# Kernel tuning notes

Hardware: AMD Instinct MI355X
Metric: run time of the kernel (lower is better)

Reference implementation:

```python
import jax, jax.numpy as jnp
import numpy as np


def lstm_encode(x, Wih, Whh, b):
    """x: [S, T, F] -> final hidden state [S, H]. PyTorch LSTM gate order (i, f, g, o)."""
    S = x.shape[0]
    H = Whh.shape[1]

    def step(carry, xt):
        h, c = carry
        z = xt @ Wih.T + h @ Whh.T + b  # [S, 4H]
        i, f, g, o = jnp.split(z, 4, axis=-1)
        c = jax.nn.sigmoid(f) * c + jax.nn.sigmoid(i) * jnp.tanh(g)
        h = jax.nn.sigmoid(o) * jnp.tanh(c)
        return (h, c), None

    init = (jnp.zeros((S, H), x.dtype), jnp.zeros((S, H), x.dtype))
    (h, _), _ = jax.lax.scan(step, init, jnp.swapaxes(x, 0, 1))
    return h


def gatv2(h, Ws, Wd, a, bias):
    """Dense GATv2 on batched fully-connected graphs (no self loops).
    h: [G, N, Hin]; Ws, Wd: [nh, Hin, O]; a: [nh, O]; bias: [nh, O] -> [G, N, nh, O].
    Graph is fully connected (all i != j), so edge-softmax == dense row softmax
    with the diagonal masked out; this is the efficient dense form of the
    gather / LeakyReLU / edge-softmax / scatter pattern in DGL's GATv2Conv."""
    nh = Ws.shape[0]
    N = h.shape[1]
    self_mask = jnp.eye(N, dtype=bool)
    outs = []
    for hd in range(nh):  # small fixed head count; loop caps peak memory
        fs = h @ Ws[hd]  # [G, N, O] source-projected feats (messages)
        fd = h @ Wd[hd]  # [G, N, O] dst-projected feats
        e = jax.nn.leaky_relu(fd[:, :, None, :] + fs[:, None, :, :], 0.2)  # [G, dst, src, O]
        logits = jnp.where(self_mask, -jnp.inf, e @ a[hd])  # [G, dst, src]
        attn = jax.nn.softmax(logits, axis=-1)
        outs.append(jnp.einsum('gds,gso->gdo', attn, fs) + bias[hd])
    return jnp.stack(outs, axis=2)


def cosine(x, y, eps=1e-6):
    xn = x / jnp.maximum(jnp.linalg.norm(x, axis=-1, keepdims=True), eps)
    yn = y / jnp.maximum(jnp.linalg.norm(y, axis=-1, keepdims=True), eps)
    return (xn * yn).sum(-1)


def setup_inputs() -> dict:
    key = jax.random.key(0)
    B, K, T, N, F, H, GH, NH = 16, 4, 64, 128, 16, 32, 32, 8
    ks = jax.random.split(key, 16)

    def rn(k, shape, scale=1.0):
        return jax.random.normal(k, shape, jnp.float32) * scale

    return {
        'anchor': rn(ks[0], (B, T, N, F)),
        'pos': rn(ks[1], (B, T, N, F)),
        'neg': rn(ks[2], (B, K, T, N, F)),
        'hideout': rn(ks[3], (B, 2)),
        'timestep': jax.random.uniform(ks[4], (B, 1), jnp.float32),
        'Wih': rn(ks[5], (4 * H, F), 1.0 / np.sqrt(F)),
        'Whh': rn(ks[6], (4 * H, H), 1.0 / np.sqrt(H)),
        'b_lstm': rn(ks[7], (4 * H,), 0.1),
        'W1s': rn(ks[8], (NH, H, H), 1.0 / np.sqrt(H)),
        'W1d': rn(ks[9], (NH, H, H), 1.0 / np.sqrt(H)),
        'a1': rn(ks[10], (NH, H), 1.0 / np.sqrt(H)),
        'b1': rn(ks[11], (NH, H), 0.1),
        'W2s': rn(ks[12], (1, H, GH), 1.0 / np.sqrt(H)),
        'W2d': rn(ks[13], (1, H, GH), 1.0 / np.sqrt(H)),
        'a2': rn(ks[14], (1, GH), 1.0 / np.sqrt(GH)),
        'b2': rn(ks[15], (1, GH), 0.1),
        'num_agents': 128,
    }


def reference(anchor, pos, neg, hideout, timestep, Wih, Whh, b_lstm,
              W1s, W1d, a1, b1, W2s, W2d, a2, b2, num_agents):
    B, T, N, F = anchor.shape
    K = neg.shape[1]
    H = Whh.shape[1]
    # per-agent time series -> LSTM sequences
    a_seq = jnp.transpose(anchor, (0, 2, 1, 3)).reshape(B * N, T, F)
    p_seq = jnp.transpose(pos, (0, 2, 1, 3)).reshape(B * N, T, F)
    n_seq = jnp.transpose(neg, (0, 1, 3, 2, 4)).reshape(B * K * N, T, F)
    hn = lstm_encode(jnp.concatenate([a_seq, p_seq, n_seq], 0), Wih, Whh, b_lstm)
    hg = hn.reshape(-1, N, H)  # [(2+K)*B, N, H] batched fully-connected graphs
    h1 = gatv2(hg, W1s, W1d, a1, b1).mean(axis=2)  # mean over 8 heads
    h2 = gatv2(h1, W2s, W2d, a2, b2)[:, :, 0, :]   # single head, squeezed
    pooled = h2.mean(axis=1)                        # AvgPooling over nodes
    anchor_res = pooled[:B]
    pos_res = pooled[B:2 * B]
    neg_res = pooled[2 * B:].reshape(B, K, -1)
    sim_pos = cosine(anchor_res, pos_res)[:, None]      # [B, 1]
    sim_neg = cosine(anchor_res[:, None, :], neg_res)   # [B, K]
    all_vecs = jnp.concatenate([sim_neg, sim_pos], axis=1)  # positive last
    contrastive = (-jax.nn.log_softmax(all_vecs, axis=1)[:, -1]).mean()
    res = jnp.concatenate([anchor_res, hideout, timestep], axis=-1)
    return res, contrastive
```

## Files before the change

kernel.cpp:

```cpp
#include <hip/hip_runtime.h>
#include <math.h>


typedef __bf16 bf16x8 __attribute__((ext_vector_type(8)));
typedef float  f32x4  __attribute__((ext_vector_type(4)));
typedef unsigned int u32x4 __attribute__((ext_vector_type(4)));

__device__ __forceinline__ float fast_rcp(float x) { return __builtin_amdgcn_rcpf(x); }
__device__ __forceinline__ float sigm(float x)     { return fast_rcp(1.f + __expf(-x)); }
__device__ __forceinline__ float tanh_fast(float x){ return fmaf(2.f, fast_rcp(1.f + __expf(-2.f * x)), -1.f); }

#define KEEP4(x) asm volatile("" : "+v"(x))

__global__ __launch_bounds__(256, 1) void lstm_mfma_kernel(
    const float* __restrict__ anchor, const float* __restrict__ pos,
    const float* __restrict__ neg, const float* __restrict__ Wih,
    const float* __restrict__ Whh, const float* __restrict__ bias,
    float* __restrict__ hn)
{
    __shared__ unsigned int Hbuf[2][2][512];
    const int tid  = threadIdx.x;
    const int pair = tid >> 7;
    const int wid  = (tid >> 6) & 1;
    const int lane = tid & 63;
    const int l15  = lane & 15;
    const int g4   = lane >> 4;

    for (int i = tid; i < 2048; i += 256) ((unsigned int*)Hbuf)[i] = 0u;

    u32x4 whhH[4], whhL[4], wihH[4];
    float bq[4];
    #pragma unroll
    for (int G = 0; G < 4; ++G) {
        const int c = G * 32 + wid * 16 + l15;
        bq[G] = bias[c];
        union { u32x4 u; bf16x8 v; } th, tl, ti;
        const float* wr = Whh + c * 32 + g4 * 8;
        #pragma unroll
        for (int i = 0; i < 8; ++i) {
            float wv = wr[i];
            __bf16 hi = (__bf16)wv;
            th.v[i] = hi;
            tl.v[i] = (__bf16)(wv - (float)hi);
        }
        if (g4 < 2) {
            const float* wr2 = Wih + c * 16 + g4 * 8;
            #pragma unroll
            for (int i = 0; i < 8; ++i) ti.v[i] = (__bf16)wr2[i];
        } else {
            #pragma unroll
            for (int i = 0; i < 8; ++i) ti.v[i] = (__bf16)0.f;
        }
        whhH[G] = th.u; whhL[G] = tl.u; wihH[G] = ti.u;
    }
    #pragma unroll
    for (int G = 0; G < 4; ++G) { KEEP4(whhH[G]); KEEP4(whhL[G]); KEEP4(wihH[G]); }

    const int s = blockIdx.x * 32 + pair * 16 + l15;
    const float* xbase; int sl;
    if (s < 2048)      { xbase = anchor; sl = s; }
    else if (s < 4096) { xbase = pos;    sl = s - 2048; }
    else               { xbase = neg;    sl = s - 4096; }
    const bool xact = (g4 < 2);
    const float* xp = xbase + (sl >> 7) * 131072 + (sl & 127) * 16 + (xact ? g4 * 8 : 0);

    const float4 z4 = make_float4(0.f, 0.f, 0.f, 0.f);
    float4 xaA = z4, xbA = z4, xaB = z4, xbB = z4;
    if (xact) {
        xaA = *(const float4*)(xp);        xbA = *(const float4*)(xp + 4);
        xaB = *(const float4*)(xp + 2048); xbB = *(const float4*)(xp + 2052);
    }

    float cst[4] = {0,0,0,0};
    float hv[4]  = {0,0,0,0};

    const int c0  = g4 * 2;
    const int swz = (l15 & 3) << 1;
    const int ro0 = l15 * 32 + ((c0 ^ swz) << 2);
    const int ro1 = l15 * 32 + (((c0 + 1) ^ swz) << 2);
    const int jw  = wid * 16 + l15;
    unsigned int* buf0 = Hbuf[pair][0];
    unsigned int* buf1 = Hbuf[pair][1];
    int cur = 0;
    __syncthreads();

    #define LSTM_STEP(XA, XB)                                                          \
    {                                                                                  \
        const unsigned int* rb = cur ? buf1 : buf0;                                    \
        unsigned int*       wb = cur ? buf0 : buf1;                                    \
        bf16x8 ax;                                                                     \
        ax[0]=(__bf16)XA.x; ax[1]=(__bf16)XA.y; ax[2]=(__bf16)XA.z; ax[3]=(__bf16)XA.w;\
        ax[4]=(__bf16)XB.x; ax[5]=(__bf16)XB.y; ax[6]=(__bf16)XB.z; ax[7]=(__bf16)XB.w;\
        uint4 v0 = *(const uint4*)(rb + ro0);                                          \
        uint4 v1 = *(const uint4*)(rb + ro1);                                          \
        union { unsigned int u[4]; bf16x8 v; } ahi;                                    \
        ahi.u[0] = __builtin_amdgcn_perm(v0.y, v0.x, 0x05040100u);                     \
        ahi.u[1] = __builtin_amdgcn_perm(v0.w, v0.z, 0x05040100u);                     \
        ahi.u[2] = __builtin_amdgcn_perm(v1.y, v1.x, 0x05040100u);                     \
        ahi.u[3] = __builtin_amdgcn_perm(v1.w, v1.z, 0x05040100u);                     \
        f32x4 z[4];                                                                    \
        _Pragma("unroll")                                                              \
        for (int G = 0; G < 4; ++G) {                                                  \
            f32x4 a = __builtin_amdgcn_mfma_f32_16x16x32_bf16(                         \
                ax, __builtin_bit_cast(bf16x8, wihH[G]), (f32x4)(0.f), 0, 0, 0);       \
            a = __builtin_amdgcn_mfma_f32_16x16x32_bf16(                               \
                ahi.v, __builtin_bit_cast(bf16x8, whhH[G]), a, 0, 0, 0);               \
            a = __builtin_amdgcn_mfma_f32_16x16x32_bf16(                               \
                ahi.v, __builtin_bit_cast(bf16x8, whhL[G]), a, 0, 0, 0);               \
            z[G] = a;                                                                  \
        }                                                                              \
        _Pragma("unroll")                                                              \
        for (int r = 0; r < 4; ++r) {                                                  \
            float zi = z[0][r] + bq[0];                                                \
            float zf = z[1][r] + bq[1];                                                \
            float zg = z[2][r] + bq[2];                                                \
            float zo = z[3][r] + bq[3];                                                \
            float cn = fmaf(sigm(zf), cst[r], sigm(zi) * tanh_fast(zg));               \
            cst[r] = cn;                                                               \
            float h = sigm(zo) * tanh_fast(cn);                                        \
            hv[r] = h;                                                                 \
            unsigned int pk = (unsigned int)__builtin_bit_cast(unsigned short,         \
                                                               (__bf16)h);            \
            const int mm = g4 * 4 + r;                                                 \
            wb[mm * 32 + (((jw >> 2) ^ ((mm & 3) << 1)) << 2) + (jw & 3)] = pk;        \
        }                                                                              \
        __syncthreads();                                                               \
        cur ^= 1;                                                                      \
    }

    for (int t = 0; t < 64; t += 2) {
        float4 cA1 = xaA, cA2 = xbA;
        if (xact && t + 2 < 64) {
            const float* p = xp + (t + 2) * 2048;
            xaA = *(const float4*)(p); xbA = *(const float4*)(p + 4);
        }
        LSTM_STEP(cA1, cA2);

        float4 cB1 = xaB, cB2 = xbB;
        if (xact && t + 3 < 64) {
            const float* p = xp + (t + 3) * 2048;
            xaB = *(const float4*)(p); xbB = *(const float4*)(p + 4);
        }
        LSTM_STEP(cB1, cB2);
    }
    #undef LSTM_STEP

    const int seq0 = blockIdx.x * 32 + pair * 16;
    #pragma unroll
    for (int r = 0; r < 4; ++r) {
        hn[(seq0 + g4 * 4 + r) * 32 + jw] = hv[r];
    }
}

__device__ __forceinline__ int fsoff(int n) { return n * 36 + ((n >> 5) << 2); }

__global__ __launch_bounds__(256) void gat1_kernel(
    const float* __restrict__ hn, const float* __restrict__ W1s,
    const float* __restrict__ W1d, const float* __restrict__ a1,
    const float* __restrict__ b1, float* __restrict__ h1heads)
{
    const int g = blockIdx.x >> 4, hd = (blockIdx.x >> 1) & 7, half = blockIdx.x & 1;
    const int dbase = half << 6;
    __shared__ float FSf[128 * 36 + 16];
    __shared__ float FD[64][36];
    __shared__ float AVr[32];
    __shared__ float As06[128];
    __shared__ float Ad06[64];
    const int tid = threadIdx.x;

    if (tid < 32) AVr[tid] = a1[hd * 32 + tid];

    {
        const int o = tid & 31, nb = tid >> 5;
        const bool own = (nb >> 2) == half;
        float wcs[32];
        const float* wsp = W1s + hd * 1024 + o;
        #pragma unroll
        for (int k = 0; k < 32; ++k) wcs[k] = wsp[k * 32];
        const float* hp = hn + g * 4096 + nb * 512;
        if (own) {
            float wcd[32];
            const float* wdp = W1d + hd * 1024 + o;
            #pragma unroll
            for (int k = 0; k < 32; ++k) wcd[k] = wdp[k * 32];
            #pragma unroll 1
            for (int n = 0; n < 16; ++n) {
                const int row = nb * 16 + n;
                float a0 = 0.f, a1_ = 0.f, b0 = 0.f, b1_ = 0.f;
                #pragma unroll
                for (int k0 = 0; k0 < 32; k0 += 4) {
                    float4 hv = *(const float4*)(hp + n * 32 + k0);
                    a0 = fmaf(hv.x, wcs[k0+0], a0); b0 = fmaf(hv.x, wcd[k0+0], b0);
                    a1_ = fmaf(hv.y, wcs[k0+1], a1_); b1_ = fmaf(hv.y, wcd[k0+1], b1_);
                    a0 = fmaf(hv.z, wcs[k0+2], a0); b0 = fmaf(hv.z, wcd[k0+2], b0);
                    a1_ = fmaf(hv.w, wcs[k0+3], a1_); b1_ = fmaf(hv.w, wcd[k0+3], b1_);
                }
                FSf[fsoff(row) + o] = a0 + a1_;
                FD[row - dbase][o] = b0 + b1_;
            }
        } else {
            #pragma unroll 1
            for (int n = 0; n < 16; ++n) {
                const int row = nb * 16 + n;
                float a0 = 0.f, a1_ = 0.f;
                #pragma unroll
                for (int k0 = 0; k0 < 32; k0 += 4) {
                    float4 hv = *(const float4*)(hp + n * 32 + k0);
                    a0 = fmaf(hv.x, wcs[k0+0], a0);
                    a1_ = fmaf(hv.y, wcs[k0+1], a1_);
                    a0 = fmaf(hv.z, wcs[k0+2], a0);
                    a1_ = fmaf(hv.w, wcs[k0+3], a1_);
                }
                FSf[fsoff(row) + o] = a0 + a1_;
            }
        }
    }
    __syncthreads();

    if (tid < 128) {
        float ss = 0.f;
        const float* fr = FSf + fsoff(tid);
        #pragma unroll
        for (int oo = 0; oo < 32; ++oo) {
            int o = (oo + tid) & 31;
            ss = fmaf(AVr[o], fr[o], ss);
        }
        As06[tid] = 0.6f * ss;
    } else if (tid < 192) {
        const int dl = tid - 128;
        float sd = 0.f;
        #pragma unroll
        for (int oo = 0; oo < 32; ++oo) {
            int o = (oo + dl) & 31;
            sd = fmaf(AVr[o], FD[dl][o], sd);
        }
        Ad06[dl] = 0.6f * sd;
    }
    __syncthreads();

    const int dl = tid >> 2, d = dbase + dl, sq = tid & 3, sbase = sq << 5;
    float fdr[32], avs[32];
    #pragma unroll
    for (int c = 0; c < 8; ++c) {
        float4 v = *(const float4*)&FD[dl][c * 4];
        fdr[c*4+0] = v.x; fdr[c*4+1] = v.y; fdr[c*4+2] = v.z; fdr[c*4+3] = v.w;
        float4 wv = *(const float4*)&AVr[c * 4];
        avs[c*4+0] = 0.4f * wv.x; avs[c*4+1] = 0.4f * wv.y;
        avs[c*4+2] = 0.4f * wv.z; avs[c*4+3] = 0.4f * wv.w;
    }
    const float adc = Ad06[dl];

    float Z = 0.f;
    float acc[32];
    #pragma unroll
    for (int o = 0; o < 32; ++o) acc[o] = 0.f;
    #pragma unroll 1
    for (int si = 0; si < 32; ++si) {
        const int s = sbase + si;
        const float* fr = FSf + fsoff(s);
        float4 fa[8];
        #pragma unroll
        for (int c = 0; c < 8; ++c) fa[c] = *(const float4*)(fr + c * 4);
        float c0 = 0.f, c1 = 0.f, c2 = 0.f, c3 = 0.f;
        #pragma unroll
        for (int c = 0; c < 8; ++c) {
            float e0 = fdr[c*4+0] + fa[c].x; c0 = fmaf(avs[c*4+0], __builtin_fabsf(e0), c0);
            float e1 = fdr[c*4+1] + fa[c].y; c1 = fmaf(avs[c*4+1], __builtin_fabsf(e1), c1);
            float e2 = fdr[c*4+2] + fa[c].z; c2 = fmaf(avs[c*4+2], __builtin_fabsf(e2), c2);
            float e3 = fdr[c*4+3] + fa[c].w; c3 = fmaf(avs[c*4+3], __builtin_fabsf(e3), c3);
        }
        float v = adc + As06[s] + ((c0 + c1) + (c2 + c3));
        float e = (s == d) ? 0.f : __expf(v);
        Z += e;
        #pragma unroll
        for (int c = 0; c < 8; ++c) {
            acc[c*4+0] = fmaf(e, fa[c].x, acc[c*4+0]);
            acc[c*4+1] = fmaf(e, fa[c].y, acc[c*4+1]);
            acc[c*4+2] = fmaf(e, fa[c].z, acc[c*4+2]);
            acc[c*4+3] = fmaf(e, fa[c].w, acc[c*4+3]);
        }
    }
    Z += __shfl_xor(Z, 1); Z += __shfl_xor(Z, 2);
    const float rz = fast_rcp(Z);
    #pragma unroll
    for (int o = 0; o < 32; ++o) {
        acc[o] += __shfl_xor(acc[o], 1);
        acc[o] += __shfl_xor(acc[o], 2);
    }

    if (sq == 0) {
        float* dst = h1heads + ((size_t)((g * 8 + hd) * 128 + d)) * 32;
        const float* bp = b1 + hd * 32;
        #pragma unroll
        for (int c = 0; c < 8; ++c) {
            float4 v;
            v.x = fmaf(acc[c*4+0], rz, bp[c*4+0]);
            v.y = fmaf(acc[c*4+1], rz, bp[c*4+1]);
            v.z = fmaf(acc[c*4+2], rz, bp[c*4+2]);
            v.w = fmaf(acc[c*4+3], rz, bp[c*4+3]);
            *(float4*)(dst + c * 4) = v;
        }
    }
}

__global__ __launch_bounds__(256) void gat2_kernel(
    const float* __restrict__ h1heads, const float* __restrict__ W2s,
    const float* __restrict__ W2d, const float* __restrict__ a2,
    const float* __restrict__ b2, float* __restrict__ pooled)
{
    const int g = blockIdx.x;
    __shared__ float HS[128][36];
    __shared__ float FSf[128 * 36 + 16];
    __shared__ float FD[128][36];
    __shared__ float AVr[32];
    __shared__ float As06[128];
    __shared__ float Ad06[128];
    const int tid = threadIdx.x;

    if (tid < 32) AVr[tid] = a2[tid];

    {
        #pragma unroll
        for (int i = 0; i < 4; ++i) {
            int idx4 = i * 256 + tid;
            float sx = 0.f, sy = 0.f, sz = 0.f, sw = 0.f;
            #pragma unroll
            for (int hdd = 0; hdd < 8; ++hdd) {
                const float4* src = (const float4*)(h1heads + (size_t)(g * 8 + hdd) * 4096);
                float4 v = src[idx4];
                sx += v.x; sy += v.y; sz += v.z; sw += v.w;
            }
            int n = idx4 >> 3, k0 = (idx4 & 7) * 4;
            float4 r; r.x = sx * 0.125f; r.y = sy * 0.125f; r.z = sz * 0.125f; r.w = sw * 0.125f;
            *(float4*)&HS[n][k0] = r;
        }
    }
    __syncthreads();

    {
        const int o = tid & 31, nb = tid >> 5;
        float wcs[32], wcd[32];
        const float* wsp = W2s + o;
        const float* wdp = W2d + o;
        #pragma unroll
        for (int k = 0; k < 32; ++k) { wcs[k] = wsp[k * 32]; wcd[k] = wdp[k * 32]; }
        #pragma unroll 1
        for (int n = nb * 16; n < nb * 16 + 16; ++n) {
            float a0 = 0.f, a1_ = 0.f, b0 = 0.f, b1_ = 0.f;
            #pragma unroll
            for (int k0 = 0; k0 < 32; k0 += 4) {
                const float4 hv = *(const float4*)&HS[n][k0];
                a0 = fmaf(hv.x, wcs[k0+0], a0); b0 = fmaf(hv.x, wcd[k0+0], b0);
                a1_ = fmaf(hv.y, wcs[k0+1], a1_); b1_ = fmaf(hv.y, wcd[k0+1], b1_);
                a0 = fmaf(hv.z, wcs[k0+2], a0); b0 = fmaf(hv.z, wcd[k0+2], b0);
                a1_ = fmaf(hv.w, wcs[k0+3], a1_); b1_ = fmaf(hv.w, wcd[k0+3], b1_);
            }
            FSf[fsoff(n) + o] = a0 + a1_;
            FD[n][o] = b0 + b1_;
        }
    }
    __syncthreads();

    if (tid < 128) {
        float ss = 0.f, sd = 0.f;
        const float* fr = FSf + fsoff(tid);
        #pragma unroll
        for (int oo = 0; oo < 32; ++oo) {
            int o = (oo + tid) & 31;
            float a = AVr[o];
            ss = fmaf(a, fr[o], ss);
            sd = fmaf(a, FD[tid][o], sd);
        }
        As06[tid] = 0.6f * ss;
        Ad06[tid] = 0.6f * sd;
    }
    __syncthreads();

    const int d = tid >> 1, sbase = (tid & 1) << 6;
    float fdr[32], avs[32];
    #pragma unroll
    for (int c = 0; c < 8; ++c) {
        float4 v = *(const float4*)&FD[d][c * 4];
        fdr[c*4+0] = v.x; fdr[c*4+1] = v.y; fdr[c*4+2] = v.z; fdr[c*4+3] = v.w;
        float4 wv = *(const float4*)&AVr[c * 4];
        avs[c*4+0] = 0.4f * wv.x; avs[c*4+1] = 0.4f * wv.y;
        avs[c*4+2] = 0.4f * wv.z; avs[c*4+3] = 0.4f * wv.w;
    }
    const float adc = Ad06[d];

    float Z = 0.f;
    float acc[32];
    #pragma unroll
    for (int o = 0; o < 32; ++o) acc[o] = 0.f;
    #pragma unroll 1
    for (int si = 0; si < 64; ++si) {
        const int s = sbase + si;
        const float* fr = FSf + fsoff(s);
        float4 fa[8];
        #pragma unroll
        for (int c = 0; c < 8; ++c) fa[c] = *(const float4*)(fr + c * 4);
        float c0 = 0.f, c1 = 0.f, c2 = 0.f, c3 = 0.f;
        #pragma unroll
        for (int c = 0; c < 8; ++c) {
            float e0 = fdr[c*4+0] + fa[c].x; c0 = fmaf(avs[c*4+0], __builtin_fabsf(e0), c0);
            float e1 = fdr[c*4+1] + fa[c].y; c1 = fmaf(avs[c*4+1], __builtin_fabsf(e1), c1);
            float e2 = fdr[c*4+2] + fa[c].z; c2 = fmaf(avs[c*4+2], __builtin_fabsf(e2), c2);
            float e3 = fdr[c*4+3] + fa[c].w; c3 = fmaf(avs[c*4+3], __builtin_fabsf(e3), c3);
        }
        float v = adc + As06[s] + ((c0 + c1) + (c2 + c3));
        float e = (s == d) ? 0.f : __expf(v);
        Z += e;
        #pragma unroll
        for (int c = 0; c < 8; ++c) {
            acc[c*4+0] = fmaf(e, fa[c].x, acc[c*4+0]);
            acc[c*4+1] = fmaf(e, fa[c].y, acc[c*4+1]);
            acc[c*4+2] = fmaf(e, fa[c].z, acc[c*4+2]);
            acc[c*4+3] = fmaf(e, fa[c].w, acc[c*4+3]);
        }
    }
    Z += __shfl_xor(Z, 1);
    const float rz = fast_rcp(Z);
    #pragma unroll
    for (int o = 0; o < 32; ++o) acc[o] += __shfl_xor(acc[o], 1);

    __syncthreads();
    if ((tid & 1) == 0) {
        #pragma unroll
        for (int c = 0; c < 4; ++c) {
            float4 v;
            v.x = acc[c*4+0] * rz; v.y = acc[c*4+1] * rz;
            v.z = acc[c*4+2] * rz; v.w = acc[c*4+3] * rz;
            *(float4*)&FD[d][c * 4] = v;
        }
    } else {
        #pragma unroll
        for (int c = 4; c < 8; ++c) {
            float4 v;
            v.x = acc[c*4+0] * rz; v.y = acc[c*4+1] * rz;
            v.z = acc[c*4+2] * rz; v.w = acc[c*4+3] * rz;
            *(float4*)&FD[d][c * 4] = v;
        }
    }
    __syncthreads();

    if (tid < 32) {
        float sp = 0.f;
        #pragma unroll 1
        for (int n = 0; n < 128; ++n) sp += FD[n][tid];
        pooled[g * 32 + tid] = fmaf(sp, 1.f / 128.f, b2[tid]);
    }
}

__global__ void final_kernel(const float* __restrict__ pooled,
                             const float* __restrict__ hideout,
                             const float* __restrict__ timestep,
                             float* __restrict__ out)
{
    const int b = threadIdx.x;
    __shared__ float lossArr[16];
    if (b < 16) {
        const float* A  = pooled + b * 32;
        const float* Pv = pooled + (16 + b) * 32;
        float av[32];
        float na = 0.f;
        #pragma unroll
        for (int i = 0; i < 32; ++i) { av[i] = A[i]; na += av[i] * av[i]; }
        float npv = 0.f, dp = 0.f;
        #pragma unroll
        for (int i = 0; i < 32; ++i) { float p = Pv[i]; npv += p * p; dp += av[i] * p; }
        const float eps = 1e-6f;
        const float ia = 1.f / fmaxf(sqrtf(na), eps);
        const float sp = dp * ia / fmaxf(sqrtf(npv), eps);
        float sn[4];
        #pragma unroll
        for (int k = 0; k < 4; ++k) {
            const float* Nv = pooled + (32 + b * 4 + k) * 32;
            float nn = 0.f, dn = 0.f;
            #pragma unroll
            for (int i = 0; i < 32; ++i) { float q = Nv[i]; nn += q * q; dn += av[i] * q; }
            sn[k] = dn * ia / fmaxf(sqrtf(nn), eps);
        }
        float m = sp;
        #pragma unroll
        for (int k = 0; k < 4; ++k) m = fmaxf(m, sn[k]);
        float Z = expf(sp - m);
        #pragma unroll
        for (int k = 0; k < 4; ++k) Z += expf(sn[k] - m);
        lossArr[b] = logf(Z) + m - sp;
        float* r = out + b * 35;
        #pragma unroll
        for (int i = 0; i < 32; ++i) r[i] = av[i];
        r[32] = hideout[b * 2];
        r[33] = hideout[b * 2 + 1];
        r[34] = timestep[b];
    }
    __syncthreads();
    if (b == 0) {
        float s = 0.f;
        #pragma unroll
        for (int i = 0; i < 16; ++i) s += lossArr[i];
        out[560] = s * (1.f / 16.f);
    }
}

extern "C" void kernel_launch(void* const* d_in, const int* in_sizes, int n_in,
                              void* d_out, int out_size, void* d_ws, size_t ws_size,
                              hipStream_t stream) {
    const float* anchor   = (const float*)d_in[0];
    const float* pos      = (const float*)d_in[1];
    const float* neg      = (const float*)d_in[2];
    const float* hideout  = (const float*)d_in[3];
    const float* timestep = (const float*)d_in[4];
    const float* Wih      = (const float*)d_in[5];
    const float* Whh      = (const float*)d_in[6];
    const float* b_lstm   = (const float*)d_in[7];
    const float* W1s      = (const float*)d_in[8];
    const float* W1d      = (const float*)d_in[9];
    const float* a1       = (const float*)d_in[10];
    const float* b1       = (const float*)d_in[11];
    const float* W2s      = (const float*)d_in[12];
    const float* W2d      = (const float*)d_in[13];
    const float* a2       = (const float*)d_in[14];
    const float* b2       = (const float*)d_in[15];
    float* out = (float*)d_out;

    char* ws = (char*)d_ws;
    float* hn      = (float*)(ws);
    float* h1heads = (float*)(ws + 1605632);
    float* pooled  = (float*)(ws + 14188544);

    hipLaunchKernelGGL(lstm_mfma_kernel, dim3(384), dim3(256), 0, stream,
                       anchor, pos, neg, Wih, Whh, b_lstm, hn);
    hipLaunchKernelGGL(gat1_kernel,  dim3(1536), dim3(256), 0, stream,
                       hn, W1s, W1d, a1, b1, h1heads);
    hipLaunchKernelGGL(gat2_kernel,  dim3(96),   dim3(256), 0, stream,
                       h1heads, W2s, W2d, a2, b2, pooled);
    hipLaunchKernelGGL(final_kernel, dim3(1),    dim3(64),  0, stream,
                       pooled, hideout, timestep, out);
}
```

Baseline: 162.1 us.

## Split LSTM blocks to one wave pair and give each GAT1 thread two destinations

The LSTM kernel now runs 128-thread blocks, each holding one pair of waves, across twice as many blocks. Its per-step __syncthreads is replaced by a raw s_barrier preceded by an LDS wait, so the two independent wave pairs that used to share a block no longer stall each other at every timestep. The GAT1 kernel stops splitting destinations into halves: each block handles one (graph, head) and computes both source and destination projections once, and each thread accumulates two destination rows. Each source-feature load is reused twice, and the redundant source projection done by both halves is removed. The cost is higher register pressure in GAT1 (two 32-wide accumulators) and fewer GAT1 blocks.

```diff
diff --git a/kernel.cpp b/kernel.cpp
--- a/kernel.cpp
+++ b/kernel.cpp
@@ -12,21 +12,28 @@
 
 #define KEEP4(x) asm volatile("" : "+v"(x))
 
-__global__ __launch_bounds__(256, 1) void lstm_mfma_kernel(
+#define PAIR_BARRIER() do {                                     \
+    asm volatile("s_waitcnt lgkmcnt(0)" ::: "memory");          \
+    __builtin_amdgcn_sched_barrier(0);                          \
+    __builtin_amdgcn_s_barrier();                               \
+    __builtin_amdgcn_sched_barrier(0);                          \
+} while (0)
+
+__global__ __launch_bounds__(128, 1) void lstm_mfma_kernel(
     const float* __restrict__ anchor, const float* __restrict__ pos,
     const float* __restrict__ neg, const float* __restrict__ Wih,
     const float* __restrict__ Whh, const float* __restrict__ bias,
     float* __restrict__ hn)
 {
-    __shared__ unsigned int Hbuf[2][2][512];
+    __shared__ unsigned int Hbuf[2][512];
     const int tid  = threadIdx.x;
-    const int pair = tid >> 7;
-    const int wid  = (tid >> 6) & 1;
+    const int wid  = tid >> 6;
     const int lane = tid & 63;
     const int l15  = lane & 15;
     const int g4   = lane >> 4;
 
-    for (int i = tid; i < 2048; i += 256) ((unsigned int*)Hbuf)[i] = 0u;
+    #pragma unroll
+    for (int i = 0; i < 8; ++i) ((unsigned int*)Hbuf)[tid + i * 128] = 0u;
 
     u32x4 whhH[4], whhL[4], wihH[4];
     float bq[4];
@@ -56,7 +63,7 @@
     #pragma unroll
     for (int G = 0; G < 4; ++G) { KEEP4(whhH[G]); KEEP4(whhL[G]); KEEP4(wihH[G]); }
 
-    const int s = blockIdx.x * 32 + pair * 16 + l15;
+    const int s = blockIdx.x * 16 + l15;
     const float* xbase; int sl;
     if (s < 2048)      { xbase = anchor; sl = s; }
     else if (s < 4096) { xbase = pos;    sl = s - 2048; }
@@ -79,15 +86,13 @@
     const int ro0 = l15 * 32 + ((c0 ^ swz) << 2);
     const int ro1 = l15 * 32 + (((c0 + 1) ^ swz) << 2);
     const int jw  = wid * 16 + l15;
-    unsigned int* buf0 = Hbuf[pair][0];
-    unsigned int* buf1 = Hbuf[pair][1];
     int cur = 0;
-    __syncthreads();
+    PAIR_BARRIER();
 
     #define LSTM_STEP(XA, XB)                                                          \
     {                                                                                  \
-        const unsigned int* rb = cur ? buf1 : buf0;                                    \
-        unsigned int*       wb = cur ? buf0 : buf1;                                    \
+        const unsigned int* rb = Hbuf[cur];                                            \
+        unsigned int*       wb = Hbuf[cur ^ 1];                                        \
         bf16x8 ax;                                                                     \
         ax[0]=(__bf16)XA.x; ax[1]=(__bf16)XA.y; ax[2]=(__bf16)XA.z; ax[3]=(__bf16)XA.w;\
         ax[4]=(__bf16)XB.x; ax[5]=(__bf16)XB.y; ax[6]=(__bf16)XB.z; ax[7]=(__bf16)XB.w;\
@@ -124,7 +129,7 @@
             const int mm = g4 * 4 + r;                                                 \
             wb[mm * 32 + (((jw >> 2) ^ ((mm & 3) << 1)) << 2) + (jw & 3)] = pk;        \
         }                                                                              \
-        __syncthreads();                                                               \
+        PAIR_BARRIER();                                                                \
         cur ^= 1;                                                                      \
     }
 
@@ -145,7 +150,7 @@
     }
     #undef LSTM_STEP
 
-    const int seq0 = blockIdx.x * 32 + pair * 16;
+    const int seq0 = blockIdx.x * 16;
     #pragma unroll
     for (int r = 0; r < 4; ++r) {
         hn[(seq0 + g4 * 4 + r) * 32 + jw] = hv[r];
@@ -154,106 +159,81 @@
 
 __device__ __forceinline__ int fsoff(int n) { return n * 36 + ((n >> 5) << 2); }
 
-__global__ __launch_bounds__(256) void gat1_kernel(
+__global__ __launch_bounds__(256, 2) void gat1_kernel(
     const float* __restrict__ hn, const float* __restrict__ W1s,
     const float* __restrict__ W1d, const float* __restrict__ a1,
     const float* __restrict__ b1, float* __restrict__ h1heads)
 {
-    const int g = blockIdx.x >> 4, hd = (blockIdx.x >> 1) & 7, half = blockIdx.x & 1;
-    const int dbase = half << 6;
+    const int g = blockIdx.x >> 3, hd = blockIdx.x & 7;
     __shared__ float FSf[128 * 36 + 16];
-    __shared__ float FD[64][36];
+    __shared__ float FD[128][36];
     __shared__ float AVr[32];
     __shared__ float As06[128];
-    __shared__ float Ad06[64];
+    __shared__ float Ad06[128];
     const int tid = threadIdx.x;
 
     if (tid < 32) AVr[tid] = a1[hd * 32 + tid];
 
     {
         const int o = tid & 31, nb = tid >> 5;
-        const bool own = (nb >> 2) == half;
-        float wcs[32];
+        float wcs[32], wcd[32];
         const float* wsp = W1s + hd * 1024 + o;
-        #pragma unroll
-        for (int k = 0; k < 32; ++k) wcs[k] = wsp[k * 32];
+        const float* wdp = W1d + hd * 1024 + o;
+        #pragma unroll
+        for (int k = 0; k < 32; ++k) { wcs[k] = wsp[k * 32]; wcd[k] = wdp[k * 32]; }
         const float* hp = hn + g * 4096 + nb * 512;
-        if (own) {
-            float wcd[32];
-            const float* wdp = W1d + hd * 1024 + o;
+        #pragma unroll 1
+        for (int n = 0; n < 16; ++n) {
+            const int row = nb * 16 + n;
+            float a0 = 0.f, a1_ = 0.f, b0 = 0.f, b1_ = 0.f;
             #pragma unroll
-            for (int k = 0; k < 32; ++k) wcd[k] = wdp[k * 32];
-            #pragma unroll 1
-            for (int n = 0; n < 16; ++n) {
-                const int row = nb * 16 + n;
-                float a0 = 0.f, a1_ = 0.f, b0 = 0.f, b1_ = 0.f;
-                #pragma unroll
-                for (int k0 = 0; k0 < 32; k0 += 4) {
-                    float4 hv = *(const float4*)(hp + n * 32 + k0);
-                    a0 = fmaf(hv.x, wcs[k0+0], a0); b0 = fmaf(hv.x, wcd[k0+0], b0);
-                    a1_ = fmaf(hv.y, wcs[k0+1], a1_); b1_ = fmaf(hv.y, wcd[k0+1], b1_);
-                    a0 = fmaf(hv.z, wcs[k0+2], a0); b0 = fmaf(hv.z, wcd[k0+2], b0);
-                    a1_ = fmaf(hv.w, wcs[k0+3], a1_); b1_ = fmaf(hv.w, wcd[k0+3], b1_);
-                }
-                FSf[fsoff(row) + o] = a0 + a1_;
-                FD[row - dbase][o] = b0 + b1_;
+            for (int k0 = 0; k0 < 32; k0 += 4) {
+                float4 hv = *(const float4*)(hp + n * 32 + k0);
+                a0 = fmaf(hv.x, wcs[k0+0], a0); b0 = fmaf(hv.x, wcd[k0+0], b0);
+                a1_ = fmaf(hv.y, wcs[k0+1], a1_); b1_ = fmaf(hv.y, wcd[k0+1], b1_);
+                a0 = fmaf(hv.z, wcs[k0+2], a0); b0 = fmaf(hv.z, wcd[k0+2], b0);
+                a1_ = fmaf(hv.w, wcs[k0+3], a1_); b1_ = fmaf(hv.w, wcd[k0+3], b1_);
             }
-        } else {
-            #pragma unroll 1
-            for (int n = 0; n < 16; ++n) {
-                const int row = nb * 16 + n;
-                float a0 = 0.f, a1_ = 0.f;
-                #pragma unroll
-                for (int k0 = 0; k0 < 32; k0 += 4) {
-                    float4 hv = *(const float4*)(hp + n * 32 + k0);
-                    a0 = fmaf(hv.x, wcs[k0+0], a0);
-                    a1_ = fmaf(hv.y, wcs[k0+1], a1_);
-                    a0 = fmaf(hv.z, wcs[k0+2], a0);
-                    a1_ = fmaf(hv.w, wcs[k0+3], a1_);
-                }
-                FSf[fsoff(row) + o] = a0 + a1_;
-            }
+            FSf[fsoff(row) + o] = a0 + a1_;
+            FD[row][o] = b0 + b1_;
         }
     }
     __syncthreads();
 
     if (tid < 128) {
-        float ss = 0.f;
+        float ss = 0.f, sd = 0.f;
         const float* fr = FSf + fsoff(tid);
         #pragma unroll
         for (int oo = 0; oo < 32; ++oo) {
             int o = (oo + tid) & 31;
-            ss = fmaf(AVr[o], fr[o], ss);
+            float a = AVr[o];
+            ss = fmaf(a, fr[o], ss);
+            sd = fmaf(a, FD[tid][o], sd);
         }
         As06[tid] = 0.6f * ss;
-    } else if (tid < 192) {
-        const int dl = tid - 128;
-        float sd = 0.f;
-        #pragma unroll
-        for (int oo = 0; oo < 32; ++oo) {
-            int o = (oo + dl) & 31;
-            sd = fmaf(AVr[o], FD[dl][o], sd);
-        }
-        Ad06[dl] = 0.6f * sd;
-    }
-    __syncthreads();
-
-    const int dl = tid >> 2, d = dbase + dl, sq = tid & 3, sbase = sq << 5;
-    float fdr[32], avs[32];
+        Ad06[tid] = 0.6f * sd;
+    }
+    __syncthreads();
+
+    const int p = tid >> 2, sq = tid & 3, sbase = sq << 5;
+    const int d0 = p, d1 = p + 64;
+    float fdr0[32], fdr1[32], avs[32];
     #pragma unroll
     for (int c = 0; c < 8; ++c) {
-        float4 v = *(const float4*)&FD[dl][c * 4];
-        fdr[c*4+0] = v.x; fdr[c*4+1] = v.y; fdr[c*4+2] = v.z; fdr[c*4+3] = v.w;
+        float4 v0 = *(const float4*)&FD[d0][c * 4];
+        fdr0[c*4+0] = v0.x; fdr0[c*4+1] = v0.y; fdr0[c*4+2] = v0.z; fdr0[c*4+3] = v0.w;
+        float4 v1 = *(const float4*)&FD[d1][c * 4];
+        fdr1[c*4+0] = v1.x; fdr1[c*4+1] = v1.y; fdr1[c*4+2] = v1.z; fdr1[c*4+3] = v1.w;
         float4 wv = *(const float4*)&AVr[c * 4];
         avs[c*4+0] = 0.4f * wv.x; avs[c*4+1] = 0.4f * wv.y;
         avs[c*4+2] = 0.4f * wv.z; avs[c*4+3] = 0.4f * wv.w;
     }
-    const float adc = Ad06[dl];
-
-    float Z = 0.f;
-    float acc[32];
-    #pragma unroll
-    for (int o = 0; o < 32; ++o) acc[o] = 0.f;
+    const float adc0 = Ad06[d0], adc1 = Ad06[d1];
+
+    float Z0 = 0.f, Z1 = 0.f;
+    float acc0[32], acc1[32];
+    #pragma unroll
+    for (int o = 0; o < 32; ++o) { acc0[o] = 0.f; acc1[o] = 0.f; }
     #pragma unroll 1
     for (int si = 0; si < 32; ++si) {
         const int s = sbase + si;
@@ -261,44 +241,66 @@
         float4 fa[8];
         #pragma unroll
         for (int c = 0; c < 8; ++c) fa[c] = *(const float4*)(fr + c * 4);
-        float c0 = 0.f, c1 = 0.f, c2 = 0.f, c3 = 0.f;
+        float c00 = 0.f, c01 = 0.f, c02 = 0.f, c03 = 0.f;
+        float c10 = 0.f, c11 = 0.f, c12 = 0.f, c13 = 0.f;
         #pragma unroll
         for (int c = 0; c < 8; ++c) {
-            float e0 = fdr[c*4+0] + fa[c].x; c0 = fmaf(avs[c*4+0], __builtin_fabsf(e0), c0);
-            float e1 = fdr[c*4+1] + fa[c].y; c1 = fmaf(avs[c*4+1], __builtin_fabsf(e1), c1);
-            float e2 = fdr[c*4+2] + fa[c].z; c2 = fmaf(avs[c*4+2], __builtin_fabsf(e2), c2);
-            float e3 = fdr[c*4+3] + fa[c].w; c3 = fmaf(avs[c*4+3], __builtin_fabsf(e3), c3);
-        }
-        float v = adc + As06[s] + ((c0 + c1) + (c2 + c3));
-        float e = (s == d) ? 0.f : __expf(v);
-        Z += e;
+            float e;
+            e = fdr0[c*4+0] + fa[c].x; c00 = fmaf(avs[c*4+0], __builtin_fabsf(e), c00);
+            e = fdr1[c*4+0] + fa[c].x; c10 = fmaf(avs[c*4+0], __builtin_fabsf(e), c10);
+            e = fdr0[c*4+1] + fa[c].y; c01 = fmaf(avs[c*4+1], __builtin_fabsf(e), c01);
+            e = fdr1[c*4+1] + fa[c].y; c11 = fmaf(avs[c*4+1], __builtin_fabsf(e), c11);
+            e = fdr0[c*4+2] + fa[c].z; c02 = fmaf(avs[c*4+2], __builtin_fabsf(e), c02);
+            e = fdr1[c*4+2] + fa[c].z; c12 = fmaf(avs[c*4+2], __builtin_fabsf(e), c12);
+            e = fdr0[c*4+3] + fa[c].w; c03 = fmaf(avs[c*4+3], __builtin_fabsf(e), c03);
+            e = fdr1[c*4+3] + fa[c].w; c13 = fmaf(avs[c*4+3], __builtin_fabsf(e), c13);
+        }
+        const float ass = As06[s];
+        float v0 = adc0 + ass + ((c00 + c01) + (c02 + c03));
+        float v1 = adc1 + ass + ((c10 + c11) + (c12 + c13));
+        float e0 = (s == d0) ? 0.f : __expf(v0);
+        float e1 = (s == d1) ? 0.f : __expf(v1);
+        Z0 += e0; Z1 += e1;
         #pragma unroll
         for (int c = 0; c < 8; ++c) {
-            acc[c*4+0] = fmaf(e, fa[c].x, acc[c*4+0]);
-            acc[c*4+1] = fmaf(e, fa[c].y, acc[c*4+1]);
-            acc[c*4+2] = fmaf(e, fa[c].z, acc[c*4+2]);
-            acc[c*4+3] = fmaf(e, fa[c].w, acc[c*4+3]);
-        }
-    }
-    Z += __shfl_xor(Z, 1); Z += __shfl_xor(Z, 2);
-    const float rz = fast_rcp(Z);
+            acc0[c*4+0] = fmaf(e0, fa[c].x, acc0[c*4+0]);
+            acc1[c*4+0] = fmaf(e1, fa[c].x, acc1[c*4+0]);
+            acc0[c*4+1] = fmaf(e0, fa[c].y, acc0[c*4+1]);
+            acc1[c*4+1] = fmaf(e1, fa[c].y, acc1[c*4+1]);
+            acc0[c*4+2] = fmaf(e0, fa[c].z, acc0[c*4+2]);
+            acc1[c*4+2] = fmaf(e1, fa[c].z, acc1[c*4+2]);
+            acc0[c*4+3] = fmaf(e0, fa[c].w, acc0[c*4+3]);
+            acc1[c*4+3] = fmaf(e1, fa[c].w, acc1[c*4+3]);
+        }
+    }
+    Z0 += __shfl_xor(Z0, 1); Z0 += __shfl_xor(Z0, 2);
+    Z1 += __shfl_xor(Z1, 1); Z1 += __shfl_xor(Z1, 2);
+    const float rz0 = fast_rcp(Z0), rz1 = fast_rcp(Z1);
     #pragma unroll
     for (int o = 0; o < 32; ++o) {
-        acc[o] += __shfl_xor(acc[o], 1);
-        acc[o] += __shfl_xor(acc[o], 2);
+        acc0[o] += __shfl_xor(acc0[o], 1);
+        acc0[o] += __shfl_xor(acc0[o], 2);
+        acc1[o] += __shfl_xor(acc1[o], 1);
+        acc1[o] += __shfl_xor(acc1[o], 2);
     }
 
     if (sq == 0) {
-        float* dst = h1heads + ((size_t)((g * 8 + hd) * 128 + d)) * 32;
         const float* bp = b1 + hd * 32;
+        float* dst0 = h1heads + ((size_t)((g * 8 + hd) * 128 + d0)) * 32;
+        float* dst1 = h1heads + ((size_t)((g * 8 + hd) * 128 + d1)) * 32;
         #pragma unroll
         for (int c = 0; c < 8; ++c) {
             float4 v;
-            v.x = fmaf(acc[c*4+0], rz, bp[c*4+0]);
-            v.y = fmaf(acc[c*4+1], rz, bp[c*4+1]);
-            v.z = fmaf(acc[c*4+2], rz, bp[c*4+2]);
-            v.w = fmaf(acc[c*4+3], rz, bp[c*4+3]);
-            *(float4*)(dst + c * 4) = v;
+            v.x = fmaf(acc0[c*4+0], rz0, bp[c*4+0]);
+            v.y = fmaf(acc0[c*4+1], rz0, bp[c*4+1]);
+            v.z = fmaf(acc0[c*4+2], rz0, bp[c*4+2]);
+            v.w = fmaf(acc0[c*4+3], rz0, bp[c*4+3]);
+            *(float4*)(dst0 + c * 4) = v;
+            v.x = fmaf(acc1[c*4+0], rz1, bp[c*4+0]);
+            v.y = fmaf(acc1[c*4+1], rz1, bp[c*4+1]);
+            v.z = fmaf(acc1[c*4+2], rz1, bp[c*4+2]);
+            v.w = fmaf(acc1[c*4+3], rz1, bp[c*4+3]);
+            *(float4*)(dst1 + c * 4) = v;
         }
     }
 }
@@ -529,9 +531,9 @@
     float* h1heads = (float*)(ws + 1605632);
     float* pooled  = (float*)(ws + 14188544);
 
-    hipLaunchKernelGGL(lstm_mfma_kernel, dim3(384), dim3(256), 0, stream,
+    hipLaunchKernelGGL(lstm_mfma_kernel, dim3(768), dim3(128), 0, stream,
                        anchor, pos, neg, Wih, Whh, b_lstm, hn);
-    hipLaunchKernelGGL(gat1_kernel,  dim3(1536), dim3(256), 0, stream,
+    hipLaunchKernelGGL(gat1_kernel,  dim3(768),  dim3(256), 0, stream,
                        hn, W1s, W1d, a1, b1, h1heads);
     hipLaunchKernelGGL(gat2_kernel,  dim3(96),   dim3(256), 0, stream,
                        h1heads, W2s, W2d, a2, b2, pooled);
```

Result: slower. 175.2 us (+8.1%).
